# Performance work log

Hardware: AMD Instinct MI355X
Metric: run time of the kernel (lower is better)

The kernel has to match this reference:

```python
import jax, jax.numpy as jnp
import numpy as np

B, S, DIM = 2, 2048, 2048
NH, NKV = 16, 8
HD = DIM // NH  # 128
ROPE_THETA = 10000.0


def setup_inputs() -> dict:
    key = jax.random.key(0)
    ks = jax.random.split(key, 7)
    std = DIM ** -0.5
    x = jax.random.normal(ks[0], (B, S, DIM), jnp.float32)
    wq = jax.random.normal(ks[1], (NH * HD, DIM), jnp.float32) * std
    wk = jax.random.normal(ks[2], (NKV * HD, DIM), jnp.float32) * std
    wv = jax.random.normal(ks[3], (NKV * HD, DIM), jnp.float32) * std
    wo = jax.random.normal(ks[4], (DIM, NH * HD), jnp.float32) * std
    inv_freq = 1.0 / (ROPE_THETA ** (jnp.arange(0, HD, 2, dtype=jnp.float32) / HD))
    ang = jnp.arange(S, dtype=jnp.float32)[:, None] * inv_freq[None, :]  # [S, HD//2]
    freqs_cos = jnp.cos(ang)
    freqs_sin = jnp.sin(ang)
    # diffusion-style random per-batch token mask: t ~ U[0,1) per batch row
    t = jax.random.uniform(ks[5], (B, 1))
    mask = jax.random.uniform(ks[6], (B, S)) < t  # True = masked key
    mask = mask.at[:, 0].set(False)  # first token never masked
    return dict(x=x, wq=wq, wk=wk, wv=wv, wo=wo,
                freqs_cos=freqs_cos, freqs_sin=freqs_sin, mask=mask)


def _rope(x, cos, sin):
    # x: [b, s, h, d]; pairs (x[2i], x[2i+1]) rotated by angle[s, i]
    xr, xi = x[..., 0::2], x[..., 1::2]
    c = cos[None, :, None, :]
    s = sin[None, :, None, :]
    out = jnp.stack([xr * c - xi * s, xr * s + xi * c], axis=-1)
    return out.reshape(x.shape)


def reference(x, wq, wk, wv, wo, freqs_cos, freqs_sin, mask):
    b, s, _ = x.shape
    xq = jnp.einsum('bsd,ed->bse', x, wq).reshape(b, s, NH, HD)
    xk = jnp.einsum('bsd,ed->bse', x, wk).reshape(b, s, NKV, HD)
    xv = jnp.einsum('bsd,ed->bse', x, wv).reshape(b, s, NKV, HD)
    xq = _rope(xq, freqs_cos, freqs_sin)
    xk = _rope(xk, freqs_cos, freqs_sin)
    n_rep = NH // NKV
    xk = jnp.repeat(xk, n_rep, axis=2)  # repeat_kv (GQA)
    xv = jnp.repeat(xv, n_rep, axis=2)
    q = xq.transpose(0, 2, 1, 3)  # [b, h, s, d]
    k = xk.transpose(0, 2, 1, 3)
    v = xv.transpose(0, 2, 1, 3)
    scale = 1.0 / np.sqrt(HD).astype(np.float32)
    scores = jnp.einsum('bhqd,bhkd->bhqk', q, k) * scale  # [b, h, s, s]
    scores = jnp.where(mask[:, None, None, :], -jnp.inf, scores)
    probs = jax.nn.softmax(scores, axis=-1)
    out = jnp.einsum('bhqk,bhkd->bhqd', probs, v)
    out = out.transpose(0, 2, 1, 3).reshape(b, s, NH * HD)
    return jnp.einsum('bse,de->bsd', out, wo)
```

## Files before the change

kernel.cpp:

```cpp
#include <hip/hip_runtime.h>
#include <hip/hip_bf16.h>
#include <cstdint>
#include <cstddef>

#define S_LEN   2048
#define NHQ     16
#define NKV_H   8
#define HD_DIM  128
#define DMODEL  2048
#define BATCH   2
#define KVD     (NKV_H * HD_DIM)
#define QKV_LD  4096

typedef float f32x4  __attribute__((ext_vector_type(4)));
typedef __bf16 bf16x8 __attribute__((ext_vector_type(8)));
typedef __bf16 bf16x4 __attribute__((ext_vector_type(4)));

__device__ __forceinline__ void gload_lds16(const __bf16* g, __bf16* l) {
    __builtin_amdgcn_global_load_lds(
        (const __attribute__((address_space(1))) void*)g,
        (__attribute__((address_space(3))) void*)l, 16, 0, 0);
}

__global__ __launch_bounds__(256)
void prep_kernel(const unsigned* __restrict__ x, int* __restrict__ flag_x,
                 const unsigned* __restrict__ fc, int* __restrict__ flag_fc,
                 const unsigned char* __restrict__ mraw,
                 unsigned char* __restrict__ mout, int n) {
    if (blockIdx.x == 0) {
        __shared__ int cnt;
        if (threadIdx.x == 0) cnt = 0;
        __syncthreads();
        int c = 0;
        for (int j = threadIdx.x; j < 1024; j += 256) {
            unsigned hw = x[j] & 0xFFFFu;
            unsigned e  = (hw >> 7) & 0xFF;
            if (hw == 0u || (e >= 118 && e <= 132)) c++;
        }
        atomicAdd(&cnt, c);
        __syncthreads();
        if (threadIdx.x == 0) *flag_x = (cnt > 512) ? 1 : 0;
    } else if (blockIdx.x == 1) {
        if (threadIdx.x == 0) *flag_fc = (fc[0] == 0x3F803F80u) ? 1 : 0;
    } else {
        __shared__ int f_bf16, f_f32, f_u8;
        if (threadIdx.x == 0) { f_bf16 = 0; f_f32 = 0; f_u8 = 0; }
        __syncthreads();
        const unsigned* dw = (const unsigned*)mraw;
        int ndw = n / 4;
        for (int j = threadIdx.x; j < ndw; j += blockDim.x) {
            unsigned v = dw[j];
            if (v == 0x00003F80u || v == 0x3F803F80u) f_bf16 = 1;
            else if (v == 0x3F800000u) f_f32 = 1;
            else if (v & 0xFFFFFFFEu) f_u8 = 1;
        }
        __syncthreads();
        int layout;
        if (f_bf16) layout = 3;
        else if (f_f32) layout = 2;
        else if (f_u8) layout = 0;
        else layout = 1;
        for (int i = threadIdx.x; i < n; i += blockDim.x) {
            unsigned v;
            if (layout == 0)      v = mraw[i];
            else if (layout == 3) v = ((const unsigned short*)mraw)[i];
            else                  v = ((const unsigned*)mraw)[i];
            mout[i] = v ? 1u : 0u;
        }
    }
}

__device__ __forceinline__ void conv8(const void* src, __bf16* dst,
                                      size_t off, int isbf16) {
    if (isbf16) {
        *reinterpret_cast<uint4*>(dst + off) =
            *reinterpret_cast<const uint4*>((const __bf16*)src + off);
    } else {
        const float* f = (const float*)src + off;
        float4 a = *reinterpret_cast<const float4*>(f);
        float4 b = *reinterpret_cast<const float4*>(f + 4);
        bf16x8 v;
        v[0] = (__bf16)a.x; v[1] = (__bf16)a.y; v[2] = (__bf16)a.z; v[3] = (__bf16)a.w;
        v[4] = (__bf16)b.x; v[5] = (__bf16)b.y; v[6] = (__bf16)b.z; v[7] = (__bf16)b.w;
        *reinterpret_cast<bf16x8*>(dst + off) = v;
    }
}

__global__ __launch_bounds__(256)
void conv_all_kernel(const void* __restrict__ x,  const void* __restrict__ wq,
                     const void* __restrict__ wk, const void* __restrict__ wv,
                     __bf16* __restrict__ xb, __bf16* __restrict__ wcomb,
                     const int* __restrict__ dflag) {
    int i = blockIdx.x * 256 + threadIdx.x;
    int isb = *dflag;
    if (i < 1048576) {
        conv8(x, xb, (size_t)i * 8, isb);
    } else if (i < 1572864) {
        conv8(wq, wcomb, (size_t)(i - 1048576) * 8, isb);
    } else if (i < 1835008) {
        conv8(wk, wcomb + (size_t)2048 * 2048, (size_t)(i - 1572864) * 8, isb);
    } else {
        conv8(wv, wcomb + (size_t)3072 * 2048, (size_t)(i - 1835008) * 8, isb);
    }
}

__global__ __launch_bounds__(256)
void conv_bf16_strided_kernel(const void* __restrict__ src,
                              __bf16* __restrict__ dstbase,
                              int n8, const int* __restrict__ dflag) {
    int i = blockIdx.x * blockDim.x + threadIdx.x;
    if (i >= n8) return;
    size_t off = (size_t)i * 8;
    size_t row = off >> 11;
    size_t col = off & 2047;
    __bf16* dst = dstbase + row * QKV_LD + col;
    if (*dflag) {
        *reinterpret_cast<uint4*>(dst) =
            *reinterpret_cast<const uint4*>((const __bf16*)src + off);
    } else {
        const float* f = (const float*)src + off;
        float4 a = *reinterpret_cast<const float4*>(f);
        float4 b = *reinterpret_cast<const float4*>(f + 4);
        bf16x8 v;
        v[0] = (__bf16)a.x; v[1] = (__bf16)a.y; v[2] = (__bf16)a.z; v[3] = (__bf16)a.w;
        v[4] = (__bf16)b.x; v[5] = (__bf16)b.y; v[6] = (__bf16)b.z; v[7] = (__bf16)b.w;
        *reinterpret_cast<bf16x8*>(dst) = v;
    }
}

template <bool OUT_BF16>
__global__ __launch_bounds__(256)
void gemm_bt_async(const __bf16* __restrict__ A, const __bf16* __restrict__ Bw,
                   void* __restrict__ Cv, int K, int lda, int ldb, int ldc) {
    __shared__ __align__(16) __bf16 As[128 * 64];
    __shared__ __align__(16) __bf16 Bs[128 * 64];

    const int t    = threadIdx.x;
    const int w    = t >> 6;
    const int lane = t & 63;
    const int quad = lane >> 4;
    const int l16  = lane & 15;
    const int wm   = (w >> 1) * 64;
    const int wn   = (w & 1) * 64;

    const int nwg  = gridDim.x * gridDim.y;
    const int lin  = blockIdx.y * gridDim.x + blockIdx.x;
    const int swz  = (lin & 7) * (nwg >> 3) + (lin >> 3);
    const int m0   = (swz % gridDim.x) * 128;
    const int n0   = (swz / gridDim.x) * 128;

    const int rl   = lane >> 3;
    const int gl   = lane & 7;

    f32x4 acc[4][4];
#pragma unroll
    for (int i = 0; i < 4; ++i)
#pragma unroll
        for (int j = 0; j < 4; ++j) acc[i][j] = (f32x4){0.f, 0.f, 0.f, 0.f};

    for (int k0 = 0; k0 < K; k0 += 64) {
        __syncthreads();
#pragma unroll
        for (int p = 0; p < 4; ++p) {
            const int rowb = w * 32 + p * 8;
            const int r    = rowb + rl;
            const int gA   = gl ^ rl;
            gload_lds16(A  + (size_t)(m0 + r) * lda + k0 + gA * 8, &As[rowb * 64]);
            gload_lds16(Bw + (size_t)(n0 + r) * ldb + k0 + gA * 8, &Bs[rowb * 64]);
        }
        __syncthreads();
#pragma unroll
        for (int ks = 0; ks < 2; ++ks) {
            const int G = ks * 4 + quad;
            const int gsw = (G ^ (l16 & 7)) * 8;
            bf16x8 af[4], bf[4];
#pragma unroll
            for (int i = 0; i < 4; ++i)
                af[i] = *reinterpret_cast<const bf16x8*>(
                    &As[(wm + i * 16 + l16) * 64 + gsw]);
#pragma unroll
            for (int j = 0; j < 4; ++j)
                bf[j] = *reinterpret_cast<const bf16x8*>(
                    &Bs[(wn + j * 16 + l16) * 64 + gsw]);
#pragma unroll
            for (int i = 0; i < 4; ++i)
#pragma unroll
                for (int j = 0; j < 4; ++j)
                    acc[i][j] = __builtin_amdgcn_mfma_f32_16x16x32_bf16(
                        af[i], bf[j], acc[i][j], 0, 0, 0);
        }
    }
#pragma unroll
    for (int i = 0; i < 4; ++i)
#pragma unroll
        for (int r = 0; r < 4; ++r) {
            size_t m = (size_t)(m0 + wm + i * 16 + quad * 4 + r);
#pragma unroll
            for (int j = 0; j < 4; ++j) {
                int n = n0 + wn + j * 16 + l16;
                if constexpr (OUT_BF16)
                    ((__hip_bfloat16*)Cv)[m * ldc + n] = __float2bfloat16(acc[i][j][r]);
                else
                    ((float*)Cv)[m * ldc + n] = acc[i][j][r];
            }
        }
}

__global__ void rope_kernel(__hip_bfloat16* __restrict__ xqk,
                            const void* __restrict__ cosv,
                            const void* __restrict__ sinv,
                            const int* __restrict__ dflag_fc,
                            int npairs) {
    int idx = blockIdx.x * blockDim.x + threadIdx.x;
    if (idx >= npairs) return;
    int i  = idx & 63;
    int h  = (idx >> 6) % 24;
    int bs = idx / (64 * 24);
    int s  = bs & (S_LEN - 1);
    float c, sn;
    if (*dflag_fc) {
        c  = __bfloat162float(((const __hip_bfloat16*)cosv)[s * 64 + i]);
        sn = __bfloat162float(((const __hip_bfloat16*)sinv)[s * 64 + i]);
    } else {
        c  = ((const float*)cosv)[s * 64 + i];
        sn = ((const float*)sinv)[s * 64 + i];
    }
    unsigned* p = (unsigned*)(xqk + (size_t)bs * QKV_LD + h * HD_DIM) + i;
    unsigned u = *p;
    float xr = __uint_as_float(u << 16);
    float xi = __uint_as_float(u & 0xFFFF0000u);
    float o0 = xr * c - xi * sn;
    float o1 = xr * sn + xi * c;
    union { __hip_bfloat16 h2[2]; unsigned u32; } out;
    out.h2[0] = __float2bfloat16(o0);
    out.h2[1] = __float2bfloat16(o1);
    *p = out.u32;
}

__global__ __launch_bounds__(256)
void transpose_v_kernel(const __hip_bfloat16* __restrict__ xv,
                        __hip_bfloat16* __restrict__ vt) {
    __shared__ unsigned short T[32][36];
    const int t  = threadIdx.x;
    const int s0 = blockIdx.x * 32;
    const int d0 = blockIdx.y * 32;
    const int z  = blockIdx.z;
    const int b  = z >> 3;
    const int kv = z & 7;
    {
        int sr = t >> 3, dc = (t & 7) * 4;
        const unsigned short* p = (const unsigned short*)xv
            + (size_t)(b * S_LEN + s0 + sr) * QKV_LD + kv * 128 + d0 + dc;
        uint2 v = *reinterpret_cast<const uint2*>(p);
        T[sr][dc + 0] = (unsigned short)(v.x & 0xFFFFu);
        T[sr][dc + 1] = (unsigned short)(v.x >> 16);
        T[sr][dc + 2] = (unsigned short)(v.y & 0xFFFFu);
        T[sr][dc + 3] = (unsigned short)(v.y >> 16);
    }
    __syncthreads();
    {
        int dr = t >> 3, sc = (t & 7) * 4;
        unsigned w0 = (unsigned)T[sc + 0][dr] | ((unsigned)T[sc + 1][dr] << 16);
        unsigned w1 = (unsigned)T[sc + 2][dr] | ((unsigned)T[sc + 3][dr] << 16);
        unsigned short* q = (unsigned short*)vt
            + ((size_t)z * 128 + d0 + dr) * S_LEN + s0 + sc;
        uint2 v; v.x = w0; v.y = w1;
        *reinterpret_cast<uint2*>(q) = v;
    }
}

__global__ __launch_bounds__(256)
void attn_mfma2_kernel(__hip_bfloat16* qkv,
                       const __hip_bfloat16* __restrict__ vt_g,
                       const unsigned char* __restrict__ msk) {
    __shared__ __align__(16) __bf16 Ks[64 * 128];
    __shared__ __align__(16) __bf16 Vt[128 * 64];
    __shared__ __align__(16) __bf16 Ps[4][32][64];

    const int t    = threadIdx.x;
    const int w    = t >> 6;
    const int lane = t & 63;
    const int quad = lane >> 4;
    const int l16  = lane & 15;

    const int bid = ((blockIdx.x & 7) << 6) | (blockIdx.x >> 3);
    const int qt  = bid & 15;
    const int h   = (bid >> 4) & (NHQ - 1);
    const int b   = bid >> 8;
    const int kvh = h >> 1;
    const int q0  = qt * 128;

    bf16x8 qf[2][4];
    {
        const __bf16* qrow = (const __bf16*)qkv
            + (size_t)(b * S_LEN + q0 + w * 32 + l16) * QKV_LD + h * 128 + quad * 8;
#pragma unroll
        for (int g = 0; g < 2; ++g)
#pragma unroll
            for (int ks = 0; ks < 4; ++ks)
                qf[g][ks] = *reinterpret_cast<const bf16x8*>(
                    qrow + (size_t)g * 16 * QKV_LD + ks * 32);
    }

    float m_r[2], l_r[2];
    f32x4 o[2][8];
#pragma unroll
    for (int g = 0; g < 2; ++g) {
        m_r[g] = -INFINITY; l_r[g] = 0.f;
#pragma unroll
        for (int d0 = 0; d0 < 8; ++d0) o[g][d0] = (f32x4){0.f, 0.f, 0.f, 0.f};
    }

    const float scale2 = 0.08838834764831845f * 1.4426950408889634f;
    const int gbase = lane & 48;

    const __bf16* kp[4];
    const __bf16* vp[4];
    {
        const __bf16* xk = (const __bf16*)qkv + 2048;
        const int krl = lane >> 4, kgl = lane & 15;
        const int vrl = lane >> 3, vgl = lane & 7;
#pragma unroll
        for (int p = 0; p < 4; ++p) {
            const int row = w * 16 + p * 4 + krl;
            kp[p] = xk + (size_t)(b * S_LEN + row) * QKV_LD
                       + kvh * 128 + (kgl ^ (row & 7)) * 8;
        }
#pragma unroll
        for (int p = 0; p < 4; ++p) {
            const int row = w * 32 + p * 8 + vrl;
            vp[p] = (const __bf16*)vt_g
                  + ((size_t)(b * NKV_H + kvh) * 128 + row) * S_LEN
                  + (vgl ^ (row & 7)) * 8;
        }
    }
    const unsigned char* mbase = msk + b * S_LEN;

    auto stage_K = [&]() {
#pragma unroll
        for (int p = 0; p < 4; ++p) {
            gload_lds16(kp[p], &Ks[(w * 16 + p * 4) * 128]);
            kp[p] += 64 * QKV_LD;
        }
    };
    auto stage_V = [&]() {
#pragma unroll
        for (int p = 0; p < 4; ++p) {
            gload_lds16(vp[p], &Vt[(w * 32 + p * 8) * 64]);
            vp[p] += 64;
        }
    };

    stage_K();
    __syncthreads();

    for (int k0 = 0; k0 < S_LEN; k0 += 64) {
        stage_V();

        unsigned mk4[4];
        {
            const unsigned* mp = (const unsigned*)(mbase + k0);
#pragma unroll
            for (int n0 = 0; n0 < 4; ++n0) mk4[n0] = mp[n0 * 4 + quad];
        }

        f32x4 sc[2][4];
#pragma unroll
        for (int g = 0; g < 2; ++g)
#pragma unroll
            for (int n0 = 0; n0 < 4; ++n0) sc[g][n0] = (f32x4){0.f, 0.f, 0.f, 0.f};
        __builtin_amdgcn_s_setprio(1);
#pragma unroll
        for (int ks = 0; ks < 4; ++ks) {
            const int G = ks * 4 + quad;
#pragma unroll
            for (int n0 = 0; n0 < 4; ++n0) {
                const int row  = n0 * 16 + l16;
                const int slot = G ^ (row & 7);
                bf16x8 kf = *reinterpret_cast<const bf16x8*>(&Ks[row * 128 + slot * 8]);
                sc[0][n0] = __builtin_amdgcn_mfma_f32_16x16x32_bf16(kf, qf[0][ks], sc[0][n0], 0, 0, 0);
                sc[1][n0] = __builtin_amdgcn_mfma_f32_16x16x32_bf16(kf, qf[1][ks], sc[1][n0], 0, 0, 0);
            }
        }
        __builtin_amdgcn_s_setprio(0);

        __syncthreads();

        if (k0 + 64 < S_LEN) stage_K();

        float rm[2];
#pragma unroll
        for (int g = 0; g < 2; ++g) {
#pragma unroll
            for (int n0 = 0; n0 < 4; ++n0)
#pragma unroll
                for (int r = 0; r < 4; ++r)
                    sc[g][n0][r] = ((mk4[n0] >> (r * 8)) & 0xFF) ? -INFINITY : sc[g][n0][r];
            float tq0 = fmaxf(fmaxf(sc[g][0][0], sc[g][0][1]), fmaxf(sc[g][0][2], sc[g][0][3]));
            float tq1 = fmaxf(fmaxf(sc[g][1][0], sc[g][1][1]), fmaxf(sc[g][1][2], sc[g][1][3]));
            float tq2 = fmaxf(fmaxf(sc[g][2][0], sc[g][2][1]), fmaxf(sc[g][2][2], sc[g][2][3]));
            float tq3 = fmaxf(fmaxf(sc[g][3][0], sc[g][3][1]), fmaxf(sc[g][3][2], sc[g][3][3]));
            float m4 = fmaxf(fmaxf(tq0, tq1), fmaxf(tq2, tq3));
            m4 = fmaxf(m4, __shfl_xor(m4, 16, 64));
            m4 = fmaxf(m4, __shfl_xor(m4, 32, 64));
            rm[g] = m4;
        }

        bool need = ((rm[0] - m_r[0]) * scale2 > 8.0f) ||
                    ((rm[1] - m_r[1]) * scale2 > 8.0f);
        if (__any((int)need)) {
#pragma unroll
            for (int g = 0; g < 2; ++g) {
                float mn = fmaxf(m_r[g], rm[g]);
                float al = exp2f((m_r[g] - mn) * scale2);
                m_r[g] = mn;
                l_r[g] *= al;
                float alq[4];
#pragma unroll
                for (int r = 0; r < 4; ++r)
                    alq[r] = __shfl(al, gbase | (quad * 4 + r), 64);
#pragma unroll
                for (int d0 = 0; d0 < 8; ++d0)
#pragma unroll
                    for (int r = 0; r < 4; ++r) o[g][d0][r] *= alq[r];
            }
        }

#pragma unroll
        for (int g = 0; g < 2; ++g) {
            float negm = -m_r[g] * scale2;
#pragma unroll
            for (int n0 = 0; n0 < 4; ++n0) {
#pragma unroll
                for (int r = 0; r < 4; ++r) {
                    float p = exp2f(fmaf(sc[g][n0][r], scale2, negm));
                    sc[g][n0][r] = p;
                    l_r[g] += p;
                }
                const int kb    = n0 * 16 + quad * 4;
                const int gran  = kb >> 3;
                const int half4 = kb & 4;
                const int slot  = gran ^ (l16 & 7);
                bf16x4 pk;
                pk[0] = (__bf16)sc[g][n0][0];
                pk[1] = (__bf16)sc[g][n0][1];
                pk[2] = (__bf16)sc[g][n0][2];
                pk[3] = (__bf16)sc[g][n0][3];
                *reinterpret_cast<bf16x4*>(&Ps[w][g * 16 + l16][slot * 8 + half4]) = pk;
            }
        }

        __builtin_amdgcn_s_setprio(1);
#pragma unroll
        for (int kk = 0; kk < 64; kk += 32) {
            const int Gp    = (kk >> 3) + quad;
            const int slotp = Gp ^ (l16 & 7);
            bf16x8 af0 = *reinterpret_cast<const bf16x8*>(&Ps[w][l16][slotp * 8]);
            bf16x8 af1 = *reinterpret_cast<const bf16x8*>(&Ps[w][16 + l16][slotp * 8]);
#pragma unroll
            for (int d0 = 0; d0 < 8; ++d0) {
                const int row  = d0 * 16 + l16;
                const int slot = Gp ^ (row & 7);
                bf16x8 bf = *reinterpret_cast<const bf16x8*>(&Vt[row * 64 + slot * 8]);
                o[0][d0] = __builtin_amdgcn_mfma_f32_16x16x32_bf16(af0, bf, o[0][d0], 0, 0, 0);
                o[1][d0] = __builtin_amdgcn_mfma_f32_16x16x32_bf16(af1, bf, o[1][d0], 0, 0, 0);
            }
        }
        __builtin_amdgcn_s_setprio(0);

        __syncthreads();
    }

    __hip_bfloat16* att = qkv;
#pragma unroll
    for (int g = 0; g < 2; ++g) {
        float ls = l_r[g];
        ls += __shfl_xor(ls, 16, 64);
        ls += __shfl_xor(ls, 32, 64);
        float invl = 1.f / ls;
        float invq[4];
#pragma unroll
        for (int r = 0; r < 4; ++r)
            invq[r] = __shfl(invl, gbase | (quad * 4 + r), 64);
#pragma unroll
        for (int d0 = 0; d0 < 8; ++d0)
#pragma unroll
            for (int r = 0; r < 4; ++r) {
                size_t row = (size_t)(b * S_LEN + q0 + w * 32 + g * 16 + quad * 4 + r);
                att[row * QKV_LD + h * 128 + d0 * 16 + l16] =
                    __float2bfloat16(o[g][d0][r] * invq[r]);
            }
    }
}

extern "C" void kernel_launch(void* const* d_in, const int* in_sizes, int n_in,
                              void* d_out, int out_size, void* d_ws, size_t ws_size,
                              hipStream_t stream) {
    const void* x  = d_in[0];
    const void* wq = d_in[1];
    const void* wk = d_in[2];
    const void* wv = d_in[3];
    const void* wo = d_in[4];
    const void* fc = d_in[5];
    const void* fs = d_in[6];
    const unsigned char* mraw = (const unsigned char*)d_in[7];

    const int M = BATCH * S_LEN;
    char* wsb = (char*)d_ws;
    int* dflag_x  = (int*)wsb;
    int* dflag_fc = (int*)(wsb + 64);
    unsigned char* mnorm = (unsigned char*)(wsb + 128);
    __hip_bfloat16* qkv = (__hip_bfloat16*)(wsb + 8192);

    char* dob = (char*)d_out;
    __bf16* xb    = (__bf16*)dob;
    __bf16* wcomb = (__bf16*)(dob + (16u << 20));
    __hip_bfloat16* vt = (__hip_bfloat16*)d_out;

    hipLaunchKernelGGL(prep_kernel, dim3(3), dim3(256), 0, stream,
                       (const unsigned*)x, dflag_x, (const unsigned*)fc, dflag_fc,
                       mraw, mnorm, BATCH * S_LEN);

    hipLaunchKernelGGL(conv_all_kernel, dim3(8192), dim3(256), 0, stream,
                       x, wq, wk, wv, xb, wcomb, dflag_x);

    hipLaunchKernelGGL((gemm_bt_async<true>), dim3(M / 128, QKV_LD / 128), dim3(256), 0, stream,
                       xb, wcomb, (void*)qkv, DMODEL, DMODEL, DMODEL, QKV_LD);

    int npairs = M * 24 * (HD_DIM / 2);
    hipLaunchKernelGGL(rope_kernel, dim3(npairs / 256), dim3(256), 0, stream,
                       qkv, fc, fs, dflag_fc, npairs);

    hipLaunchKernelGGL(transpose_v_kernel, dim3(S_LEN / 32, HD_DIM / 32, BATCH * NKV_H),
                       dim3(256), 0, stream, qkv + 3072, vt);

    hipLaunchKernelGGL(attn_mfma2_kernel, dim3(BATCH * NHQ * (S_LEN / 128)), dim3(256), 0, stream,
                       qkv, vt, mnorm);

    hipLaunchKernelGGL(conv_bf16_strided_kernel, dim3((DMODEL * DMODEL / 8) / 256), dim3(256), 0, stream,
                       wo, (__bf16*)qkv + 2048, DMODEL * DMODEL / 8, dflag_x);

    hipLaunchKernelGGL((gemm_bt_async<false>), dim3(M / 128, DMODEL / 128), dim3(256), 0, stream,
                       (const __bf16*)qkv, (const __bf16*)qkv + 2048, d_out,
                       DMODEL, QKV_LD, QKV_LD, DMODEL);
}
```

Baseline: 455.3 us.

## Fuse RoPE into QKV GEMM, fold prep into conversion, double-buffer attention tiles

```diff
diff --git a/kernel.cpp b/kernel.cpp
--- a/kernel.cpp
+++ b/kernel.cpp
@@ -22,52 +22,18 @@
         (__attribute__((address_space(3))) void*)l, 16, 0, 0);
 }
 
-__global__ __launch_bounds__(256)
-void prep_kernel(const unsigned* __restrict__ x, int* __restrict__ flag_x,
-                 const unsigned* __restrict__ fc, int* __restrict__ flag_fc,
-                 const unsigned char* __restrict__ mraw,
-                 unsigned char* __restrict__ mout, int n) {
-    if (blockIdx.x == 0) {
-        __shared__ int cnt;
-        if (threadIdx.x == 0) cnt = 0;
-        __syncthreads();
-        int c = 0;
-        for (int j = threadIdx.x; j < 1024; j += 256) {
-            unsigned hw = x[j] & 0xFFFFu;
-            unsigned e  = (hw >> 7) & 0xFF;
-            if (hw == 0u || (e >= 118 && e <= 132)) c++;
-        }
-        atomicAdd(&cnt, c);
-        __syncthreads();
-        if (threadIdx.x == 0) *flag_x = (cnt > 512) ? 1 : 0;
-    } else if (blockIdx.x == 1) {
-        if (threadIdx.x == 0) *flag_fc = (fc[0] == 0x3F803F80u) ? 1 : 0;
-    } else {
-        __shared__ int f_bf16, f_f32, f_u8;
-        if (threadIdx.x == 0) { f_bf16 = 0; f_f32 = 0; f_u8 = 0; }
-        __syncthreads();
-        const unsigned* dw = (const unsigned*)mraw;
-        int ndw = n / 4;
-        for (int j = threadIdx.x; j < ndw; j += blockDim.x) {
-            unsigned v = dw[j];
-            if (v == 0x00003F80u || v == 0x3F803F80u) f_bf16 = 1;
-            else if (v == 0x3F800000u) f_f32 = 1;
-            else if (v & 0xFFFFFFFEu) f_u8 = 1;
-        }
-        __syncthreads();
-        int layout;
-        if (f_bf16) layout = 3;
-        else if (f_f32) layout = 2;
-        else if (f_u8) layout = 0;
-        else layout = 1;
-        for (int i = threadIdx.x; i < n; i += blockDim.x) {
-            unsigned v;
-            if (layout == 0)      v = mraw[i];
-            else if (layout == 3) v = ((const unsigned short*)mraw)[i];
-            else                  v = ((const unsigned*)mraw)[i];
-            mout[i] = v ? 1u : 0u;
-        }
-    }
+__device__ __forceinline__ int sniff_bf16(const unsigned* buf, int* cntp) {
+    if (threadIdx.x == 0) *cntp = 0;
+    __syncthreads();
+    int c = 0;
+    for (int j = threadIdx.x; j < 1024; j += 256) {
+        unsigned hw = buf[j] & 0xFFFFu;
+        unsigned e  = (hw >> 7) & 0xFF;
+        if (hw == 0u || (e >= 118 && e <= 132)) c++;
+    }
+    atomicAdd(cntp, c);
+    __syncthreads();
+    return *cntp > 512;
 }
 
 __device__ __forceinline__ void conv8(const void* src, __bf16* dst,
@@ -90,9 +56,43 @@
 void conv_all_kernel(const void* __restrict__ x,  const void* __restrict__ wq,
                      const void* __restrict__ wk, const void* __restrict__ wv,
                      __bf16* __restrict__ xb, __bf16* __restrict__ wcomb,
-                     const int* __restrict__ dflag) {
+                     const unsigned* __restrict__ fc, int* __restrict__ dflag_fc,
+                     const unsigned char* __restrict__ mraw,
+                     unsigned char* __restrict__ mout, int nmask) {
+    __shared__ int sh[4];
+    if (blockIdx.x == 8192) {
+        if (threadIdx.x == 0) *dflag_fc = (fc[0] == 0x3F803F80u) ? 1 : 0;
+        return;
+    }
+    if (blockIdx.x == 8193) {
+        __shared__ int f_bf16, f_f32, f_u8;
+        if (threadIdx.x == 0) { f_bf16 = 0; f_f32 = 0; f_u8 = 0; }
+        __syncthreads();
+        const unsigned* dw = (const unsigned*)mraw;
+        int ndw = nmask / 4;
+        for (int j = threadIdx.x; j < ndw; j += blockDim.x) {
+            unsigned v = dw[j];
+            if (v == 0x00003F80u || v == 0x3F803F80u) f_bf16 = 1;
+            else if (v == 0x3F800000u) f_f32 = 1;
+            else if (v & 0xFFFFFFFEu) f_u8 = 1;
+        }
+        __syncthreads();
+        int layout;
+        if (f_bf16) layout = 3;
+        else if (f_f32) layout = 2;
+        else if (f_u8) layout = 0;
+        else layout = 1;
+        for (int i = threadIdx.x; i < nmask; i += blockDim.x) {
+            unsigned v;
+            if (layout == 0)      v = mraw[i];
+            else if (layout == 3) v = ((const unsigned short*)mraw)[i];
+            else                  v = ((const unsigned*)mraw)[i];
+            mout[i] = v ? 1u : 0u;
+        }
+        return;
+    }
+    int isb = sniff_bf16((const unsigned*)x, &sh[0]);
     int i = blockIdx.x * 256 + threadIdx.x;
-    int isb = *dflag;
     if (i < 1048576) {
         conv8(x, xb, (size_t)i * 8, isb);
     } else if (i < 1572864) {
@@ -106,15 +106,16 @@
 
 __global__ __launch_bounds__(256)
 void conv_bf16_strided_kernel(const void* __restrict__ src,
-                              __bf16* __restrict__ dstbase,
-                              int n8, const int* __restrict__ dflag) {
+                              __bf16* __restrict__ dstbase, int n8) {
+    __shared__ int cnt;
+    int isb = sniff_bf16((const unsigned*)src, &cnt);
     int i = blockIdx.x * blockDim.x + threadIdx.x;
     if (i >= n8) return;
     size_t off = (size_t)i * 8;
     size_t row = off >> 11;
     size_t col = off & 2047;
     __bf16* dst = dstbase + row * QKV_LD + col;
-    if (*dflag) {
+    if (isb) {
         *reinterpret_cast<uint4*>(dst) =
             *reinterpret_cast<const uint4*>((const __bf16*)src + off);
     } else {
@@ -128,10 +129,12 @@
     }
 }
 
-template <bool OUT_BF16>
+template <bool OUT_BF16, bool ROPE>
 __global__ __launch_bounds__(256)
 void gemm_bt_async(const __bf16* __restrict__ A, const __bf16* __restrict__ Bw,
-                   void* __restrict__ Cv, int K, int lda, int ldb, int ldc) {
+                   void* __restrict__ Cv, int K, int lda, int ldb, int ldc,
+                   const void* __restrict__ cosv, const void* __restrict__ sinv,
+                   const int* __restrict__ dflag_fc) {
     __shared__ __align__(16) __bf16 As[128 * 64];
     __shared__ __align__(16) __bf16 Bs[128 * 64];
 
@@ -190,51 +193,39 @@
                         af[i], bf[j], acc[i][j], 0, 0, 0);
         }
     }
+
+    bool fcb = false;
+    if constexpr (ROPE) fcb = (*dflag_fc != 0);
 #pragma unroll
     for (int i = 0; i < 4; ++i)
 #pragma unroll
         for (int r = 0; r < 4; ++r) {
             size_t m = (size_t)(m0 + wm + i * 16 + quad * 4 + r);
+            const int spos = (int)(m & (S_LEN - 1));
 #pragma unroll
             for (int j = 0; j < 4; ++j) {
                 int n = n0 + wn + j * 16 + l16;
+                float v = acc[i][j][r];
+                if (ROPE && (n0 + wn + j * 16 < 3072)) {
+                    int pair = (n & 127) >> 1;
+                    float c, s;
+                    if (fcb) {
+                        c = __bfloat162float(((const __hip_bfloat16*)cosv)[spos * 64 + pair]);
+                        s = __bfloat162float(((const __hip_bfloat16*)sinv)[spos * 64 + pair]);
+                    } else {
+                        c = ((const float*)cosv)[spos * 64 + pair];
+                        s = ((const float*)sinv)[spos * 64 + pair];
+                    }
+                    float partner = __shfl_xor(v, 1, 64);
+                    float ssgn = (n & 1) ? s : -s;
+                    v = fmaf(v, c, partner * ssgn);
+                }
                 if constexpr (OUT_BF16)
-                    ((__hip_bfloat16*)Cv)[m * ldc + n] = __float2bfloat16(acc[i][j][r]);
+                    ((__hip_bfloat16*)Cv)[m * ldc + n] = __float2bfloat16(v);
                 else
-                    ((float*)Cv)[m * ldc + n] = acc[i][j][r];
+                    ((float*)Cv)[m * ldc + n] = v;
             }
         }
-}
-
-__global__ void rope_kernel(__hip_bfloat16* __restrict__ xqk,
-                            const void* __restrict__ cosv,
-                            const void* __restrict__ sinv,
-                            const int* __restrict__ dflag_fc,
-                            int npairs) {
-    int idx = blockIdx.x * blockDim.x + threadIdx.x;
-    if (idx >= npairs) return;
-    int i  = idx & 63;
-    int h  = (idx >> 6) % 24;
-    int bs = idx / (64 * 24);
-    int s  = bs & (S_LEN - 1);
-    float c, sn;
-    if (*dflag_fc) {
-        c  = __bfloat162float(((const __hip_bfloat16*)cosv)[s * 64 + i]);
-        sn = __bfloat162float(((const __hip_bfloat16*)sinv)[s * 64 + i]);
-    } else {
-        c  = ((const float*)cosv)[s * 64 + i];
-        sn = ((const float*)sinv)[s * 64 + i];
-    }
-    unsigned* p = (unsigned*)(xqk + (size_t)bs * QKV_LD + h * HD_DIM) + i;
-    unsigned u = *p;
-    float xr = __uint_as_float(u << 16);
-    float xi = __uint_as_float(u & 0xFFFF0000u);
-    float o0 = xr * c - xi * sn;
-    float o1 = xr * sn + xi * c;
-    union { __hip_bfloat16 h2[2]; unsigned u32; } out;
-    out.h2[0] = __float2bfloat16(o0);
-    out.h2[1] = __float2bfloat16(o1);
-    *p = out.u32;
 }
 
 __global__ __launch_bounds__(256)
@@ -269,13 +260,13 @@
     }
 }
 
-__global__ __launch_bounds__(256)
+__global__ __launch_bounds__(128)
 void attn_mfma2_kernel(__hip_bfloat16* qkv,
                        const __hip_bfloat16* __restrict__ vt_g,
                        const unsigned char* __restrict__ msk) {
-    __shared__ __align__(16) __bf16 Ks[64 * 128];
-    __shared__ __align__(16) __bf16 Vt[128 * 64];
-    __shared__ __align__(16) __bf16 Ps[4][32][64];
+    __shared__ __align__(16) __bf16 Ks[2][64 * 128];
+    __shared__ __align__(16) __bf16 Vt[2][128 * 64];
+    __shared__ __align__(16) __bf16 Ps[2][32][64];
 
     const int t    = threadIdx.x;
     const int w    = t >> 6;
@@ -283,12 +274,12 @@
     const int quad = lane >> 4;
     const int l16  = lane & 15;
 
-    const int bid = ((blockIdx.x & 7) << 6) | (blockIdx.x >> 3);
-    const int qt  = bid & 15;
-    const int h   = (bid >> 4) & (NHQ - 1);
-    const int b   = bid >> 8;
+    const int bid = ((blockIdx.x & 7) << 7) | (blockIdx.x >> 3);
+    const int qt  = bid & 31;
+    const int h   = (bid >> 5) & (NHQ - 1);
+    const int b   = bid >> 9;
     const int kvh = h >> 1;
-    const int q0  = qt * 128;
+    const int q0  = qt * 64;
 
     bf16x8 qf[2][4];
     {
@@ -314,21 +305,21 @@
     const float scale2 = 0.08838834764831845f * 1.4426950408889634f;
     const int gbase = lane & 48;
 
-    const __bf16* kp[4];
-    const __bf16* vp[4];
+    const __bf16* kp[8];
+    const __bf16* vp[8];
     {
         const __bf16* xk = (const __bf16*)qkv + 2048;
         const int krl = lane >> 4, kgl = lane & 15;
         const int vrl = lane >> 3, vgl = lane & 7;
 #pragma unroll
-        for (int p = 0; p < 4; ++p) {
-            const int row = w * 16 + p * 4 + krl;
+        for (int p = 0; p < 8; ++p) {
+            const int row = w * 32 + p * 4 + krl;
             kp[p] = xk + (size_t)(b * S_LEN + row) * QKV_LD
                        + kvh * 128 + (kgl ^ (row & 7)) * 8;
         }
 #pragma unroll
-        for (int p = 0; p < 4; ++p) {
-            const int row = w * 32 + p * 8 + vrl;
+        for (int p = 0; p < 8; ++p) {
+            const int row = w * 64 + p * 8 + vrl;
             vp[p] = (const __bf16*)vt_g
                   + ((size_t)(b * NKV_H + kvh) * 128 + row) * S_LEN
                   + (vgl ^ (row & 7)) * 8;
@@ -336,30 +327,25 @@
     }
     const unsigned char* mbase = msk + b * S_LEN;
 
-    auto stage_K = [&]() {
-#pragma unroll
-        for (int p = 0; p < 4; ++p) {
-            gload_lds16(kp[p], &Ks[(w * 16 + p * 4) * 128]);
+    auto stage = [&](int sb) {
+#pragma unroll
+        for (int p = 0; p < 8; ++p) {
+            gload_lds16(kp[p], &Ks[sb][(w * 32 + p * 4) * 128]);
             kp[p] += 64 * QKV_LD;
         }
+#pragma unroll
+        for (int p = 0; p < 8; ++p) {
+            gload_lds16(vp[p], &Vt[sb][(w * 64 + p * 8) * 64]);
+            vp[p] += 64;
+        }
     };
-    auto stage_V = [&]() {
-#pragma unroll
-        for (int p = 0; p < 4; ++p) {
-            gload_lds16(vp[p], &Vt[(w * 32 + p * 8) * 64]);
-            vp[p] += 64;
-        }
-    };
-
-    stage_K();
-    __syncthreads();
-
-    for (int k0 = 0; k0 < S_LEN; k0 += 64) {
-        stage_V();
+
+    auto tile_body = [&](int kmask, int cb, int sb, bool do_stage) {
+        if (do_stage) stage(sb);
 
         unsigned mk4[4];
         {
-            const unsigned* mp = (const unsigned*)(mbase + k0);
+            const unsigned* mp = (const unsigned*)(mbase + kmask);
 #pragma unroll
             for (int n0 = 0; n0 < 4; ++n0) mk4[n0] = mp[n0 * 4 + quad];
         }
@@ -377,16 +363,12 @@
             for (int n0 = 0; n0 < 4; ++n0) {
                 const int row  = n0 * 16 + l16;
                 const int slot = G ^ (row & 7);
-                bf16x8 kf = *reinterpret_cast<const bf16x8*>(&Ks[row * 128 + slot * 8]);
+                bf16x8 kf = *reinterpret_cast<const bf16x8*>(&Ks[cb][row * 128 + slot * 8]);
                 sc[0][n0] = __builtin_amdgcn_mfma_f32_16x16x32_bf16(kf, qf[0][ks], sc[0][n0], 0, 0, 0);
                 sc[1][n0] = __builtin_amdgcn_mfma_f32_16x16x32_bf16(kf, qf[1][ks], sc[1][n0], 0, 0, 0);
             }
         }
         __builtin_amdgcn_s_setprio(0);
-
-        __syncthreads();
-
-        if (k0 + 64 < S_LEN) stage_K();
 
         float rm[2];
 #pragma unroll
@@ -461,7 +443,7 @@
             for (int d0 = 0; d0 < 8; ++d0) {
                 const int row  = d0 * 16 + l16;
                 const int slot = Gp ^ (row & 7);
-                bf16x8 bf = *reinterpret_cast<const bf16x8*>(&Vt[row * 64 + slot * 8]);
+                bf16x8 bf = *reinterpret_cast<const bf16x8*>(&Vt[cb][row * 64 + slot * 8]);
                 o[0][d0] = __builtin_amdgcn_mfma_f32_16x16x32_bf16(af0, bf, o[0][d0], 0, 0, 0);
                 o[1][d0] = __builtin_amdgcn_mfma_f32_16x16x32_bf16(af1, bf, o[1][d0], 0, 0, 0);
             }
@@ -469,6 +451,14 @@
         __builtin_amdgcn_s_setprio(0);
 
         __syncthreads();
+    };
+
+    stage(0);
+    __syncthreads();
+
+    for (int k0 = 0; k0 < S_LEN; k0 += 128) {
+        tile_body(k0,      0, 1, true);
+        tile_body(k0 + 64, 1, 0, k0 + 128 < S_LEN);
     }
 
     __hip_bfloat16* att = qkv;
@@ -507,7 +497,6 @@
 
     const int M = BATCH * S_LEN;
     char* wsb = (char*)d_ws;
-    int* dflag_x  = (int*)wsb;
     int* dflag_fc = (int*)(wsb + 64);
     unsigned char* mnorm = (unsigned char*)(wsb + 128);
     __hip_bfloat16* qkv = (__hip_bfloat16*)(wsb + 8192);
@@ -517,30 +506,25 @@
     __bf16* wcomb = (__bf16*)(dob + (16u << 20));
     __hip_bfloat16* vt = (__hip_bfloat16*)d_out;
 
-    hipLaunchKernelGGL(prep_kernel, dim3(3), dim3(256), 0, stream,
-                       (const unsigned*)x, dflag_x, (const unsigned*)fc, dflag_fc,
-                       mraw, mnorm, BATCH * S_LEN);
-
-    hipLaunchKernelGGL(conv_all_kernel, dim3(8192), dim3(256), 0, stream,
-                       x, wq, wk, wv, xb, wcomb, dflag_x);
-
-    hipLaunchKernelGGL((gemm_bt_async<true>), dim3(M / 128, QKV_LD / 128), dim3(256), 0, stream,
-                       xb, wcomb, (void*)qkv, DMODEL, DMODEL, DMODEL, QKV_LD);
-
-    int npairs = M * 24 * (HD_DIM / 2);
-    hipLaunchKernelGGL(rope_kernel, dim3(npairs / 256), dim3(256), 0, stream,
-                       qkv, fc, fs, dflag_fc, npairs);
+    hipLaunchKernelGGL(conv_all_kernel, dim3(8194), dim3(256), 0, stream,
+                       x, wq, wk, wv, xb, wcomb,
+                       (const unsigned*)fc, dflag_fc, mraw, mnorm, BATCH * S_LEN);
+
+    hipLaunchKernelGGL((gemm_bt_async<true, true>), dim3(M / 128, QKV_LD / 128), dim3(256), 0, stream,
+                       xb, wcomb, (void*)qkv, DMODEL, DMODEL, DMODEL, QKV_LD,
+                       fc, fs, dflag_fc);
 
     hipLaunchKernelGGL(transpose_v_kernel, dim3(S_LEN / 32, HD_DIM / 32, BATCH * NKV_H),
                        dim3(256), 0, stream, qkv + 3072, vt);
 
-    hipLaunchKernelGGL(attn_mfma2_kernel, dim3(BATCH * NHQ * (S_LEN / 128)), dim3(256), 0, stream,
+    hipLaunchKernelGGL(attn_mfma2_kernel, dim3(BATCH * NHQ * (S_LEN / 64)), dim3(128), 0, stream,
                        qkv, vt, mnorm);
 
     hipLaunchKernelGGL(conv_bf16_strided_kernel, dim3((DMODEL * DMODEL / 8) / 256), dim3(256), 0, stream,
-                       wo, (__bf16*)qkv + 2048, DMODEL * DMODEL / 8, dflag_x);
-
-    hipLaunchKernelGGL((gemm_bt_async<false>), dim3(M / 128, DMODEL / 128), dim3(256), 0, stream,
+                       wo, (__bf16*)qkv + 2048, DMODEL * DMODEL / 8);
+
+    hipLaunchKernelGGL((gemm_bt_async<false, false>), dim3(M / 128, DMODEL / 128), dim3(256), 0, stream,
                        (const __bf16*)qkv, (const __bf16*)qkv + 2048, d_out,
-                       DMODEL, QKV_LD, QKV_LD, DMODEL);
-}
+                       DMODEL, QKV_LD, QKV_LD, DMODEL,
+                       nullptr, nullptr, nullptr);
+}
```

After: 455.9 us. No clear change (+0.1%).
